# Kernel optimization log

Measured on AMD Instinct MI355X. Metric: run time of the kernel, lower is better.

Reference implementation:

```python
import jax, jax.numpy as jnp
import numpy as np
from jax import lax

K = 20  # number of propagation steps (init kwarg k)


def _conv(x, w, padding):
    return lax.conv_general_dilated(
        x, w, window_strides=(1, 1), padding=padding,
        dimension_numbers=('NCHW', 'OIHW', 'NCHW'))


def _max_pool3(v):
    # 3x3 max pool, stride 1, SAME padding (pad value -inf like torch MaxPool2d)
    return lax.reduce_window(v, -jnp.inf, lax.max,
                             (1, 1, 3, 3), (1, 1, 1, 1), 'SAME')


def setup_inputs() -> dict:
    key = jax.random.key(0)
    k1, k2, k3, k4 = jax.random.split(key, 4)
    B, H, W = 16, 256, 256
    image = jax.random.uniform(k1, (B, 2, H, W), dtype=jnp.float32)
    # conv params, kaiming-ish scale
    W_h = jax.random.normal(k2, (150, 1, 3, 3), dtype=jnp.float32) * (1.0 / 3.0)
    b_h = jax.random.normal(k3, (150,), dtype=jnp.float32) * 0.1
    W_p = jax.random.normal(k4, (1, 150, 1, 1), dtype=jnp.float32) * (1.0 / np.sqrt(150.0))
    return {"image": image, "W_h": W_h, "b_h": b_h, "W_p": W_p}


def reference(image, W_h, b_h, W_p):
    occ = image[:, 0:1, :, :]  # [B,1,H,W] occupancy / free-space channel
    r = image[:, 1:2, :, :]    # [B,1,H,W] reward channel

    h = jax.nn.relu(_conv(occ, W_h, 'SAME') + b_h[None, :, None, None])  # [B,150,H,W]
    p = jax.nn.sigmoid(_conv(h, W_p, 'VALID'))                            # [B,1,H,W]

    def step(v, _):
        v = jnp.maximum(v, r + p * (_max_pool3(v) - r))
        return v, None

    v, _ = lax.scan(step, r, None, length=K)
    v = jnp.where(occ > 0.49, v, -jnp.ones_like(v))
    return v
```

## Files before the change

### kernel.cpp

```cpp
#include <hip/hip_runtime.h>
#include <hip/hip_bf16.h>
#include <math.h>


#define SENT -1e30f

typedef short short8 __attribute__((ext_vector_type(8)));
typedef float f32x16 __attribute__((ext_vector_type(16)));

__device__ __forceinline__ short bfb(float f) {
    __hip_bfloat16 h = __float2bfloat16(f);
    ushort u; __builtin_memcpy(&u, &h, 2);
    return (short)u;
}

__global__ __launch_bounds__(256) void conv_p_mfma(
    const float* __restrict__ image, const float* __restrict__ Wh,
    const float* __restrict__ bh, const float* __restrict__ Wp,
    float* __restrict__ pout)
{
    const int tid  = threadIdx.x;
    const int wv   = tid >> 6;
    const int lane = tid & 63;
    const int half = lane >> 5;
    const int col0 = lane & 31;
    const int b    = blockIdx.z;
    const int y    = blockIdx.x * 4 + wv;
    const float* occ = image + (size_t)b * 131072;

    __shared__ __align__(16) float lds_wp[160];
    if (tid < 160) lds_wp[tid] = (tid < 150) ? Wp[tid] : 0.f;
    __syncthreads();

    short8 afr0, afr1, afr2, afr3, afr4;
#define BUILD_A(AFR, G)                                                      \
    {                                                                        \
        int ch = 32 * (G) + col0;                                            \
        bool ok = ch < 150;                                                  \
        int cs = ok ? ch : 0;                                                \
        float w0 = ok ? Wh[cs*9+0] : 0.f, w1 = ok ? Wh[cs*9+1] : 0.f;        \
        float w2 = ok ? Wh[cs*9+2] : 0.f, w3 = ok ? Wh[cs*9+3] : 0.f;        \
        float w4 = ok ? Wh[cs*9+4] : 0.f, w5 = ok ? Wh[cs*9+5] : 0.f;        \
        float w6 = ok ? Wh[cs*9+6] : 0.f, w7 = ok ? Wh[cs*9+7] : 0.f;        \
        float w8 = ok ? Wh[cs*9+8] : 0.f, bb = ok ? bh[cs]     : 0.f;        \
        AFR[0] = half ? bfb(w8) : bfb(w0);                                   \
        AFR[1] = half ? bfb(bb) : bfb(w1);                                   \
        AFR[2] = half ? (short)0 : bfb(w2);                                  \
        AFR[3] = half ? (short)0 : bfb(w3);                                  \
        AFR[4] = half ? (short)0 : bfb(w4);                                  \
        AFR[5] = half ? (short)0 : bfb(w5);                                  \
        AFR[6] = half ? (short)0 : bfb(w6);                                  \
        AFR[7] = half ? (short)0 : bfb(w7);                                  \
    }
    BUILD_A(afr0, 0) BUILD_A(afr1, 1) BUILD_A(afr2, 2)
    BUILD_A(afr3, 3) BUILD_A(afr4, 4)
#undef BUILD_A

    const f32x16 kZero = {};
    const short  kOne  = (short)0x3F80;

    float cur0, cur1, cur2, nxt0, nxt1, nxt2;
    {
        int cc = lane - 1;
        bool cok = (lane < 34) & (cc >= 0);
        cur0 = (cok & (y >= 1))   ? occ[(y - 1) * 256 + cc] : 0.f;
        cur1 = cok                ? occ[y * 256 + cc]       : 0.f;
        cur2 = (cok & (y <= 254)) ? occ[(y + 1) * 256 + cc] : 0.f;
    }

    for (int x0 = 0; x0 < 256; x0 += 32) {
        if (x0 < 224) {
            int cc = x0 + 31 + lane;
            bool cok = (lane < 34) & (cc < 256);
            nxt0 = (cok & (y >= 1))   ? occ[(y - 1) * 256 + cc] : 0.f;
            nxt1 = cok                ? occ[y * 256 + cc]       : 0.f;
            nxt2 = (cok & (y <= 254)) ? occ[(y + 1) * 256 + cc] : 0.f;
        } else { nxt0 = 0.f; nxt1 = 0.f; nxt2 = 0.f; }

        float t0 = __shfl(cur0, col0), t1 = __shfl(cur0, col0 + 1), t2 = __shfl(cur0, col0 + 2);
        float t3 = __shfl(cur1, col0), t4 = __shfl(cur1, col0 + 1), t5 = __shfl(cur1, col0 + 2);
        float t6 = __shfl(cur2, col0), t7 = __shfl(cur2, col0 + 1), t8 = __shfl(cur2, col0 + 2);

        short8 bfr;
        bfr[0] = half ? bfb(t8) : bfb(t0);
        bfr[1] = half ? kOne    : bfb(t1);
        bfr[2] = half ? (short)0 : bfb(t2);
        bfr[3] = half ? (short)0 : bfb(t3);
        bfr[4] = half ? (short)0 : bfb(t4);
        bfr[5] = half ? (short)0 : bfb(t5);
        bfr[6] = half ? (short)0 : bfb(t6);
        bfr[7] = half ? (short)0 : bfb(t7);

        f32x16 d0 = __builtin_amdgcn_mfma_f32_32x32x16_bf16(afr0, bfr, kZero, 0, 0, 0);
        f32x16 d1 = __builtin_amdgcn_mfma_f32_32x32x16_bf16(afr1, bfr, kZero, 0, 0, 0);
        f32x16 d2 = __builtin_amdgcn_mfma_f32_32x32x16_bf16(afr2, bfr, kZero, 0, 0, 0);
        f32x16 d3 = __builtin_amdgcn_mfma_f32_32x32x16_bf16(afr3, bfr, kZero, 0, 0, 0);
        f32x16 d4 = __builtin_amdgcn_mfma_f32_32x32x16_bf16(afr4, bfr, kZero, 0, 0, 0);

        float s0 = 0.f, s1 = 0.f, s2 = 0.f, s3 = 0.f;
#define RED(D, G)                                                            \
    {                                                                        \
        const float4 wA = *(const float4*)&lds_wp[32 * (G) + 0  + 4 * half]; \
        const float4 wB = *(const float4*)&lds_wp[32 * (G) + 8  + 4 * half]; \
        const float4 wC = *(const float4*)&lds_wp[32 * (G) + 16 + 4 * half]; \
        const float4 wD = *(const float4*)&lds_wp[32 * (G) + 24 + 4 * half]; \
        s0 = fmaf(wA.x, fmaxf(D[0],  0.f), s0);                              \
        s1 = fmaf(wA.y, fmaxf(D[1],  0.f), s1);                              \
        s2 = fmaf(wA.z, fmaxf(D[2],  0.f), s2);                              \
        s3 = fmaf(wA.w, fmaxf(D[3],  0.f), s3);                              \
        s0 = fmaf(wB.x, fmaxf(D[4],  0.f), s0);                              \
        s1 = fmaf(wB.y, fmaxf(D[5],  0.f), s1);                              \
        s2 = fmaf(wB.z, fmaxf(D[6],  0.f), s2);                              \
        s3 = fmaf(wB.w, fmaxf(D[7],  0.f), s3);                              \
        s0 = fmaf(wC.x, fmaxf(D[8],  0.f), s0);                              \
        s1 = fmaf(wC.y, fmaxf(D[9],  0.f), s1);                              \
        s2 = fmaf(wC.z, fmaxf(D[10], 0.f), s2);                              \
        s3 = fmaf(wC.w, fmaxf(D[11], 0.f), s3);                              \
        s0 = fmaf(wD.x, fmaxf(D[12], 0.f), s0);                              \
        s1 = fmaf(wD.y, fmaxf(D[13], 0.f), s1);                              \
        s2 = fmaf(wD.z, fmaxf(D[14], 0.f), s2);                              \
        s3 = fmaf(wD.w, fmaxf(D[15], 0.f), s3);                              \
    }
        RED(d0, 0) RED(d1, 1) RED(d2, 2) RED(d3, 3) RED(d4, 4)
#undef RED

        float s = (s0 + s1) + (s2 + s3);
        s += __shfl_xor(s, 32);

        float p = 1.f / (1.f + __expf(-s));
        if (lane < 32)
            pout[(size_t)b * 65536 + y * 256 + x0 + lane] = p;

        cur0 = nxt0; cur1 = nxt1; cur2 = nxt2;
    }
}

__global__ __launch_bounds__(512, 2) void mvprop_kernel(
    const float* __restrict__ image, const float* __restrict__ pbuf,
    float* __restrict__ out)
{
    const int tid  = threadIdx.x;
    const int w    = tid >> 6;
    const int lane = tid & 63;
    const int b    = blockIdx.z;
    const int gy0  = blockIdx.y * 16 - 20;
    const int x4   = lane * 4;

    const float* rimg = image + (size_t)b * 131072 + 65536;
    const float* pp   = pbuf  + (size_t)b * 65536;

    float v[7][4], r[7][4], p[7][4];
#pragma unroll
    for (int i = 0; i < 7; ++i) {
        int gy = gy0 + w * 7 + i;
        if (gy >= 0 && gy < 256) {
            float4 rv = *(const float4*)&rimg[gy * 256 + x4];
            float4 pv = *(const float4*)&pp[gy * 256 + x4];
            r[i][0] = rv.x; r[i][1] = rv.y; r[i][2] = rv.z; r[i][3] = rv.w;
            p[i][0] = pv.x; p[i][1] = pv.y; p[i][2] = pv.z; p[i][3] = pv.w;
        } else {
            r[i][0] = r[i][1] = r[i][2] = r[i][3] = SENT;
            p[i][0] = p[i][1] = p[i][2] = p[i][3] = 0.f;
        }
        v[i][0] = r[i][0]; v[i][1] = r[i][1];
        v[i][2] = r[i][2]; v[i][3] = r[i][3];
    }

    __shared__ float4 gT[2][8][64];
    __shared__ float4 gB[2][8][64];

    for (int t = 0; t < 20; ++t) {
        int bf = t & 1;
        gT[bf][w][lane] = make_float4(v[0][0], v[0][1], v[0][2], v[0][3]);
        gB[bf][w][lane] = make_float4(v[6][0], v[6][1], v[6][2], v[6][3]);
        __syncthreads();
        float4 abv = (w > 0) ? gB[bf][w - 1][lane]
                             : make_float4(SENT, SENT, SENT, SENT);
        float4 blw = (w < 7) ? gT[bf][w + 1][lane]
                             : make_float4(SENT, SENT, SENT, SENT);

        float pv0 = abv.x, pv1 = abv.y, pv2 = abv.z, pv3 = abv.w;
#pragma unroll
        for (int i = 0; i < 7; ++i) {
            float c0 = v[i][0], c1 = v[i][1], c2 = v[i][2], c3 = v[i][3];
            float n0, n1, n2, n3;
            if (i < 6) { n0 = v[i+1][0]; n1 = v[i+1][1]; n2 = v[i+1][2]; n3 = v[i+1][3]; }
            else       { n0 = blw.x;     n1 = blw.y;     n2 = blw.z;     n3 = blw.w;     }
            float vm0 = fmaxf(pv0, fmaxf(c0, n0));
            float vm1 = fmaxf(pv1, fmaxf(c1, n1));
            float vm2 = fmaxf(pv2, fmaxf(c2, n2));
            float vm3 = fmaxf(pv3, fmaxf(c3, n3));
            float lL = __shfl_up(vm3, 1);
            lL = (lane == 0) ? SENT : lL;
            float rR = __shfl_down(vm0, 1);
            rR = (lane == 63) ? SENT : rR;
            float h0 = fmaxf(lL,  fmaxf(vm0, vm1));
            float h1 = fmaxf(vm0, fmaxf(vm1, vm2));
            float h2 = fmaxf(vm1, fmaxf(vm2, vm3));
            float h3 = fmaxf(vm2, fmaxf(vm3, rR));
            v[i][0] = fmaxf(c0, fmaf(p[i][0], h0 - r[i][0], r[i][0]));
            v[i][1] = fmaxf(c1, fmaf(p[i][1], h1 - r[i][1], r[i][1]));
            v[i][2] = fmaxf(c2, fmaf(p[i][2], h2 - r[i][2], r[i][2]));
            v[i][3] = fmaxf(c3, fmaf(p[i][3], h3 - r[i][3], r[i][3]));
            pv0 = c0; pv1 = c1; pv2 = c2; pv3 = c3;
        }
    }

    const float* occ = image + (size_t)b * 131072;
#pragma unroll
    for (int i = 0; i < 7; ++i) {
        int e = w * 7 + i;
        if (e >= 20 && e < 36) {
            int gy = gy0 + e;
            float4 ov = *(const float4*)&occ[gy * 256 + x4];
            float4 o;
            o.x = (ov.x > 0.49f) ? v[i][0] : -1.f;
            o.y = (ov.y > 0.49f) ? v[i][1] : -1.f;
            o.z = (ov.z > 0.49f) ? v[i][2] : -1.f;
            o.w = (ov.w > 0.49f) ? v[i][3] : -1.f;
            *(float4*)&out[(size_t)b * 65536 + gy * 256 + x4] = o;
        }
    }
}

extern "C" void kernel_launch(void* const* d_in, const int* in_sizes, int n_in,
                              void* d_out, int out_size, void* d_ws, size_t ws_size,
                              hipStream_t stream) {
    const float* image = (const float*)d_in[0];
    const float* Wh    = (const float*)d_in[1];
    const float* bh    = (const float*)d_in[2];
    const float* Wp    = (const float*)d_in[3];
    float* out  = (float*)d_out;
    float* pbuf = (float*)d_ws;

    conv_p_mfma<<<dim3(64, 1, 16), dim3(256), 0, stream>>>(image, Wh, bh, Wp, pbuf);
    mvprop_kernel<<<dim3(1, 16, 16), dim3(512), 0, stream>>>(image, pbuf, out);
}
```

Before: 60.15 us.

## Split conv kernel per 32-column tile and prepack MFMA weight fragments

The conv/sigmoid kernel no longer loops over eight 32-column tiles per wave. It launches eight times more blocks, each wave handling one tile. The bf16 A-fragments for the 3x3 weights and bias are built once by a tiny new pre-kernel into workspace and loaded as uint4 per lane, and B-fragments use packed v_cvt_pk_bf16_f32. This raises parallelism and occupancy and removes redundant per-block weight conversion, at the cost of an extra launch and lost overlap of prefetched loads.

```diff
diff --git a/kernel.cpp b/kernel.cpp
--- a/kernel.cpp
+++ b/kernel.cpp
@@ -8,16 +8,52 @@
 typedef short short8 __attribute__((ext_vector_type(8)));
 typedef float f32x16 __attribute__((ext_vector_type(16)));
 
-__device__ __forceinline__ short bfb(float f) {
+__device__ __forceinline__ uint32_t pkbf(float lo, float hi) {
+    uint32_t r;
+    asm("v_cvt_pk_bf16_f32 %0, %1, %2" : "=v"(r) : "v"(lo), "v"(hi));
+    return r;
+}
+
+__device__ __forceinline__ uint32_t bfu(float f) {
     __hip_bfloat16 h = __float2bfloat16(f);
     ushort u; __builtin_memcpy(&u, &h, 2);
-    return (short)u;
-}
-
-__global__ __launch_bounds__(256) void conv_p_mfma(
-    const float* __restrict__ image, const float* __restrict__ Wh,
-    const float* __restrict__ bh, const float* __restrict__ Wp,
-    float* __restrict__ pout)
+    return (uint32_t)u;
+}
+
+__global__ void pack_a_kernel(const float* __restrict__ Wh,
+                              const float* __restrict__ bh,
+                              uint4* __restrict__ wsA)
+{
+    const int lane = threadIdx.x;
+    const int half = lane >> 5;
+    const int col0 = lane & 31;
+#pragma unroll
+    for (int g = 0; g < 5; ++g) {
+        int ch = 32 * g + col0;
+        bool ok = ch < 150;
+        int cs = ok ? ch : 0;
+        float w0 = ok ? Wh[cs*9+0] : 0.f, w1 = ok ? Wh[cs*9+1] : 0.f;
+        float w2 = ok ? Wh[cs*9+2] : 0.f, w3 = ok ? Wh[cs*9+3] : 0.f;
+        float w4 = ok ? Wh[cs*9+4] : 0.f, w5 = ok ? Wh[cs*9+5] : 0.f;
+        float w6 = ok ? Wh[cs*9+6] : 0.f, w7 = ok ? Wh[cs*9+7] : 0.f;
+        float w8 = ok ? Wh[cs*9+8] : 0.f, bb = ok ? bh[cs]     : 0.f;
+        uint4 q;
+        if (half) {
+            q.x = (bfu(bb) << 16) | bfu(w8);
+            q.y = 0; q.z = 0; q.w = 0;
+        } else {
+            q.x = (bfu(w1) << 16) | bfu(w0);
+            q.y = (bfu(w3) << 16) | bfu(w2);
+            q.z = (bfu(w5) << 16) | bfu(w4);
+            q.w = (bfu(w7) << 16) | bfu(w6);
+        }
+        wsA[g * 64 + lane] = q;
+    }
+}
+
+__global__ __launch_bounds__(256, 4) void conv_p_mfma(
+    const float* __restrict__ image, const float* __restrict__ Wp,
+    const uint4* __restrict__ wsA, float* __restrict__ pout)
 {
     const int tid  = threadIdx.x;
     const int wv   = tid >> 6;
@@ -25,79 +61,48 @@
     const int half = lane >> 5;
     const int col0 = lane & 31;
     const int b    = blockIdx.z;
-    const int y    = blockIdx.x * 4 + wv;
+    const int y    = blockIdx.y * 4 + wv;
+    const int x0   = blockIdx.x * 32;
     const float* occ = image + (size_t)b * 131072;
+
+    uint4 q0 = wsA[0 * 64 + lane];
+    uint4 q1 = wsA[1 * 64 + lane];
+    uint4 q2 = wsA[2 * 64 + lane];
+    uint4 q3 = wsA[3 * 64 + lane];
+    uint4 q4 = wsA[4 * 64 + lane];
+
+    int cc = x0 - 1 + lane;
+    bool cok = (lane < 34) & (cc >= 0) & (cc < 256);
+    float r0 = (cok & (y >= 1))   ? occ[(y - 1) * 256 + cc] : 0.f;
+    float r1 = cok                ? occ[y * 256 + cc]       : 0.f;
+    float r2 = (cok & (y <= 254)) ? occ[(y + 1) * 256 + cc] : 0.f;
 
     __shared__ __align__(16) float lds_wp[160];
     if (tid < 160) lds_wp[tid] = (tid < 150) ? Wp[tid] : 0.f;
     __syncthreads();
 
-    short8 afr0, afr1, afr2, afr3, afr4;
-#define BUILD_A(AFR, G)                                                      \
-    {                                                                        \
-        int ch = 32 * (G) + col0;                                            \
-        bool ok = ch < 150;                                                  \
-        int cs = ok ? ch : 0;                                                \
-        float w0 = ok ? Wh[cs*9+0] : 0.f, w1 = ok ? Wh[cs*9+1] : 0.f;        \
-        float w2 = ok ? Wh[cs*9+2] : 0.f, w3 = ok ? Wh[cs*9+3] : 0.f;        \
-        float w4 = ok ? Wh[cs*9+4] : 0.f, w5 = ok ? Wh[cs*9+5] : 0.f;        \
-        float w6 = ok ? Wh[cs*9+6] : 0.f, w7 = ok ? Wh[cs*9+7] : 0.f;        \
-        float w8 = ok ? Wh[cs*9+8] : 0.f, bb = ok ? bh[cs]     : 0.f;        \
-        AFR[0] = half ? bfb(w8) : bfb(w0);                                   \
-        AFR[1] = half ? bfb(bb) : bfb(w1);                                   \
-        AFR[2] = half ? (short)0 : bfb(w2);                                  \
-        AFR[3] = half ? (short)0 : bfb(w3);                                  \
-        AFR[4] = half ? (short)0 : bfb(w4);                                  \
-        AFR[5] = half ? (short)0 : bfb(w5);                                  \
-        AFR[6] = half ? (short)0 : bfb(w6);                                  \
-        AFR[7] = half ? (short)0 : bfb(w7);                                  \
-    }
-    BUILD_A(afr0, 0) BUILD_A(afr1, 1) BUILD_A(afr2, 2)
-    BUILD_A(afr3, 3) BUILD_A(afr4, 4)
-#undef BUILD_A
+    float t0 = __shfl(r0, col0), t1 = __shfl(r0, col0 + 1), t2 = __shfl(r0, col0 + 2);
+    float t3 = __shfl(r1, col0), t4 = __shfl(r1, col0 + 1), t5 = __shfl(r1, col0 + 2);
+    float t6 = __shfl(r2, col0), t7 = __shfl(r2, col0 + 1), t8 = __shfl(r2, col0 + 2);
+
+    union { uint32_t u[4]; short8 s; } bb;
+    bb.u[0] = half ? pkbf(t8, 1.0f) : pkbf(t0, t1);
+    bb.u[1] = half ? 0u : pkbf(t2, t3);
+    bb.u[2] = half ? 0u : pkbf(t4, t5);
+    bb.u[3] = half ? 0u : pkbf(t6, t7);
+    short8 bfr = bb.s;
+
+    union { uint4 q; short8 s; } ua0, ua1, ua2, ua3, ua4;
+    ua0.q = q0; ua1.q = q1; ua2.q = q2; ua3.q = q3; ua4.q = q4;
 
     const f32x16 kZero = {};
-    const short  kOne  = (short)0x3F80;
-
-    float cur0, cur1, cur2, nxt0, nxt1, nxt2;
-    {
-        int cc = lane - 1;
-        bool cok = (lane < 34) & (cc >= 0);
-        cur0 = (cok & (y >= 1))   ? occ[(y - 1) * 256 + cc] : 0.f;
-        cur1 = cok                ? occ[y * 256 + cc]       : 0.f;
-        cur2 = (cok & (y <= 254)) ? occ[(y + 1) * 256 + cc] : 0.f;
-    }
-
-    for (int x0 = 0; x0 < 256; x0 += 32) {
-        if (x0 < 224) {
-            int cc = x0 + 31 + lane;
-            bool cok = (lane < 34) & (cc < 256);
-            nxt0 = (cok & (y >= 1))   ? occ[(y - 1) * 256 + cc] : 0.f;
-            nxt1 = cok                ? occ[y * 256 + cc]       : 0.f;
-            nxt2 = (cok & (y <= 254)) ? occ[(y + 1) * 256 + cc] : 0.f;
-        } else { nxt0 = 0.f; nxt1 = 0.f; nxt2 = 0.f; }
-
-        float t0 = __shfl(cur0, col0), t1 = __shfl(cur0, col0 + 1), t2 = __shfl(cur0, col0 + 2);
-        float t3 = __shfl(cur1, col0), t4 = __shfl(cur1, col0 + 1), t5 = __shfl(cur1, col0 + 2);
-        float t6 = __shfl(cur2, col0), t7 = __shfl(cur2, col0 + 1), t8 = __shfl(cur2, col0 + 2);
-
-        short8 bfr;
-        bfr[0] = half ? bfb(t8) : bfb(t0);
-        bfr[1] = half ? kOne    : bfb(t1);
-        bfr[2] = half ? (short)0 : bfb(t2);
-        bfr[3] = half ? (short)0 : bfb(t3);
-        bfr[4] = half ? (short)0 : bfb(t4);
-        bfr[5] = half ? (short)0 : bfb(t5);
-        bfr[6] = half ? (short)0 : bfb(t6);
-        bfr[7] = half ? (short)0 : bfb(t7);
-
-        f32x16 d0 = __builtin_amdgcn_mfma_f32_32x32x16_bf16(afr0, bfr, kZero, 0, 0, 0);
-        f32x16 d1 = __builtin_amdgcn_mfma_f32_32x32x16_bf16(afr1, bfr, kZero, 0, 0, 0);
-        f32x16 d2 = __builtin_amdgcn_mfma_f32_32x32x16_bf16(afr2, bfr, kZero, 0, 0, 0);
-        f32x16 d3 = __builtin_amdgcn_mfma_f32_32x32x16_bf16(afr3, bfr, kZero, 0, 0, 0);
-        f32x16 d4 = __builtin_amdgcn_mfma_f32_32x32x16_bf16(afr4, bfr, kZero, 0, 0, 0);
-
-        float s0 = 0.f, s1 = 0.f, s2 = 0.f, s3 = 0.f;
+    f32x16 d0 = __builtin_amdgcn_mfma_f32_32x32x16_bf16(ua0.s, bfr, kZero, 0, 0, 0);
+    f32x16 d1 = __builtin_amdgcn_mfma_f32_32x32x16_bf16(ua1.s, bfr, kZero, 0, 0, 0);
+    f32x16 d2 = __builtin_amdgcn_mfma_f32_32x32x16_bf16(ua2.s, bfr, kZero, 0, 0, 0);
+    f32x16 d3 = __builtin_amdgcn_mfma_f32_32x32x16_bf16(ua3.s, bfr, kZero, 0, 0, 0);
+    f32x16 d4 = __builtin_amdgcn_mfma_f32_32x32x16_bf16(ua4.s, bfr, kZero, 0, 0, 0);
+
+    float s0 = 0.f, s1 = 0.f, s2 = 0.f, s3 = 0.f;
 #define RED(D, G)                                                            \
     {                                                                        \
         const float4 wA = *(const float4*)&lds_wp[32 * (G) + 0  + 4 * half]; \
@@ -121,18 +126,15 @@
         s2 = fmaf(wD.z, fmaxf(D[14], 0.f), s2);                              \
         s3 = fmaf(wD.w, fmaxf(D[15], 0.f), s3);                              \
     }
-        RED(d0, 0) RED(d1, 1) RED(d2, 2) RED(d3, 3) RED(d4, 4)
+    RED(d0, 0) RED(d1, 1) RED(d2, 2) RED(d3, 3) RED(d4, 4)
 #undef RED
 
-        float s = (s0 + s1) + (s2 + s3);
-        s += __shfl_xor(s, 32);
-
-        float p = 1.f / (1.f + __expf(-s));
-        if (lane < 32)
-            pout[(size_t)b * 65536 + y * 256 + x0 + lane] = p;
-
-        cur0 = nxt0; cur1 = nxt1; cur2 = nxt2;
-    }
+    float s = (s0 + s1) + (s2 + s3);
+    s += __shfl_xor(s, 32);
+
+    float p = 1.f / (1.f + __expf(-s));
+    if (lane < 32)
+        pout[(size_t)b * 65536 + y * 256 + x0 + lane] = p;
 }
 
 __global__ __launch_bounds__(512, 2) void mvprop_kernel(
@@ -232,7 +234,9 @@
     const float* Wp    = (const float*)d_in[3];
     float* out  = (float*)d_out;
     float* pbuf = (float*)d_ws;
-
-    conv_p_mfma<<<dim3(64, 1, 16), dim3(256), 0, stream>>>(image, Wh, bh, Wp, pbuf);
+    uint4* wsA  = (uint4*)((char*)d_ws + (4 << 20));
+
+    pack_a_kernel<<<1, 64, 0, stream>>>(Wh, bh, wsA);
+    conv_p_mfma<<<dim3(8, 64, 16), dim3(256), 0, stream>>>(image, Wp, wsA, pbuf);
     mvprop_kernel<<<dim3(1, 16, 16), dim3(512), 0, stream>>>(image, pbuf, out);
 }
```

New measurement: 53.43 us. -11.2%, faster.
